# Performance work log

Hardware: AMD Instinct MI355X
Metric: run time of the kernel (lower is better)

## Reference

```python
import jax, jax.numpy as jnp
import numpy as np

TWO_PI = 2.0 * np.pi
ALPHA = 0.65
KSIZE = (3, 3, 3)   # (kOr, kH, kW)
ITERS = 1
BN_EPS = 1e-5


def _interp(v, dy, dx):
    """Bilinear sample of v[b,c,o, y+dy[o], x+dx[o]], border-clamped.
    v: [B,C,Or,H,W]; dy, dx: [Or] float per-orientation constant shifts."""
    H, W = v.shape[3], v.shape[4]
    y0 = jnp.floor(dy); fy = dy - y0; y0 = y0.astype(jnp.int32)
    iy = jnp.arange(H)[None, :] + y0[:, None]                      # [Or,H]
    g0 = jnp.take_along_axis(v, jnp.clip(iy, 0, H - 1)[None, None, :, :, None], axis=3)
    g1 = jnp.take_along_axis(v, jnp.clip(iy + 1, 0, H - 1)[None, None, :, :, None], axis=3)
    fyb = fy[None, None, :, None, None]
    v = (1.0 - fyb) * g0 + fyb * g1
    x0 = jnp.floor(dx); fx = dx - x0; x0 = x0.astype(jnp.int32)
    ix = jnp.arange(W)[None, :] + x0[:, None]                      # [Or,W]
    h0 = jnp.take_along_axis(v, jnp.clip(ix, 0, W - 1)[None, None, :, None, :], axis=4)
    h1 = jnp.take_along_axis(v, jnp.clip(ix + 1, 0, W - 1)[None, None, :, None, :], axis=4)
    fxb = fx[None, None, :, None, None]
    return (1.0 - fxb) * h0 + fxb * h1


def _convection(u, g0):
    """out[b,c,p] = u[b,c, p . g0[c]^{-1}] via trilinear resampling.
    Sample point: ((x,y) - R(theta - th0)@(x0,y0), theta - th0), theta periodic."""
    Or = u.shape[2]
    def one(uc, g):  # uc: [B,Or,H,W], g = (x0, y0, th0)
        x0, y0, th0 = g[0], g[1], g[2]
        t = th0 * Or / TWO_PI
        i = jnp.floor(t); f = t - i; i = i.astype(jnp.int32)
        # periodic linear interpolation along orientation axis
        v = (1.0 - f) * jnp.roll(uc, i, axis=1) + f * jnp.roll(uc, i + 1, axis=1)
        a = jnp.arange(Or, dtype=u.dtype) * (TWO_PI / Or) - th0
        dx = -(jnp.cos(a) * x0 - jnp.sin(a) * y0)
        dy = -(jnp.sin(a) * x0 + jnp.cos(a) * y0)
        return _interp(v[:, None], dy, dx)[:, 0]
    return jax.vmap(one, in_axes=(1, 0), out_axes=1)(u, g0)


def _se2_log(qx, qy, dth):
    """Exact SE(2) logarithm coordinates (c1,c2,c3) of group offset (qx,qy,dth)."""
    if abs(dth) < 1e-9:
        return qx, qy, dth
    h = 0.5 * dth
    cot = np.cos(h) / np.sin(h)
    return h * (qx * cot + qy), h * (-qx + qy * cot), dth


def _morph(u, metric, dilate):
    """Fractional morphological dilation (max of u(p.q) - k(q)) or erosion
    (min of u(p.q) + k(q)) with left-invariant Riemannian kernel
    k_c(q) = nu_a * d_c(q)^{2a/(2a-1)}, d_c^2 = (m0*c1)^2+(m1*c2)^2+(m2*c3)^2."""
    kOr, kH, kW = KSIZE
    Or = u.shape[2]
    thetas = jnp.arange(Or, dtype=u.dtype) * (TWO_PI / Or)
    p = 2.0 * ALPHA / (2.0 * ALPHA - 1.0)
    nu = (2.0 * ALPHA - 1.0) * (2.0 * ALPHA) ** (-p)
    out = None
    for qt in range(-(kOr // 2), kOr // 2 + 1):
        dth = qt * TWO_PI / Or
        for qy in range(-(kH // 2), kH // 2 + 1):
            for qx in range(-(kW // 2), kW // 2 + 1):
                c1, c2, c3 = _se2_log(float(qx), float(qy), dth)
                s = (metric[:, 0] * c1) ** 2 + (metric[:, 1] * c2) ** 2 + (metric[:, 2] * c3) ** 2
                k = nu * s ** (p / 2.0)                       # [C]
                # left-invariant shift: spatial offset rotated by theta_o
                dxo = jnp.cos(thetas) * qx - jnp.sin(thetas) * qy
                dyo = jnp.sin(thetas) * qx + jnp.cos(thetas) * qy
                val = _interp(jnp.roll(u, -qt, axis=2), dyo, dxo)
                kb = k[None, :, None, None, None]
                cand = val - kb if dilate else val + kb
                if out is None:
                    out = cand
                else:
                    out = jnp.maximum(out, cand) if dilate else jnp.minimum(out, cand)
    return out


def setup_inputs() -> dict:
    key = jax.random.key(0)
    ks = jax.random.split(key, 5)
    B, Cin, Cout, Or, H, W = 4, 8, 16, 8, 128, 128
    x = jax.random.normal(ks[0], (B, Cin, Or, H, W), dtype=jnp.float32)
    g0 = 0.5 * jax.random.normal(ks[1], (Cin, 3), dtype=jnp.float32)
    lo, hi = 1.4 / 3.0, 0.7 * 3.0   # reset_parameters range for metric params
    metric_dil = jax.random.uniform(ks[2], (Cin, 3), minval=lo, maxval=hi, dtype=jnp.float32)
    metric_ero = jax.random.uniform(ks[3], (Cin, 3), minval=lo, maxval=hi, dtype=jnp.float32)
    bound = 0.25  # kaiming_uniform(a=sqrt(5)) bound for [8,16] weight
    weight = jax.random.uniform(ks[4], (Cin, Cout), minval=-bound, maxval=bound, dtype=jnp.float32)
    gamma = jnp.ones((Cout,), jnp.float32)
    beta = jnp.zeros((Cout,), jnp.float32)
    return dict(x=x, g0=g0, metric_dil=metric_dil, metric_ero=metric_ero,
                weight=weight, gamma=gamma, beta=beta)


def reference(x, g0, metric_dil, metric_ero, weight, gamma, beta):
    u = x
    for _ in range(ITERS):
        u = _convection(u, g0)
        u = _morph(u, metric_dil, dilate=True)
        u = _morph(u, metric_ero, dilate=False)
    # channel mixing: [B,Cin,Or,H,W] x [Cin,Cout] -> [B,Cout,Or,H,W]
    y = jnp.einsum('bcohw,cd->bdohw', u, weight)
    # BatchNorm3d (training mode): per-channel stats over (B,Or,H,W)
    m = y.mean(axis=(0, 2, 3, 4), keepdims=True)
    v = y.var(axis=(0, 2, 3, 4), keepdims=True)
    yh = (y - m) * jax.lax.rsqrt(v + BN_EPS)
    return yh * gamma[None, :, None, None, None] + beta[None, :, None, None, None]
```

## Files before the change

### kernel.cpp

```cpp
#include <hip/hip_runtime.h>
#include <math.h>
#include <utility>

#define B 4
#define CIN 8
#define COUT 16
#define OR_ 8
#define H_ 128
#define W_ 128
#define HW 16384
#define PLANE HW
#define CH_STR (OR_*HW)
#define BATCH_STR (CIN*CH_STR)
#define NELEM (B*BATCH_STR)
#define NPOS (B*OR_*HW)
#define NB_RED 512

#define TILE 16
#define CBR 24
#define CB_S 29
#define CB_PL (CBR*CB_S)
#define DBR 20
#define DB_S 21
#define DB_PL (DBR*DB_S)

typedef __attribute__((ext_vector_type(4))) float f4;

struct Tables {
  float kdil[CIN][27];
  float kero[CIN][27];
  int   o1[CIN][OR_], o2[CIN][OR_];
  int   iy0[CIN][OR_], ix0[CIN][OR_];
  float w00[CIN][OR_], w01[CIN][OR_], w10[CIN][OR_], w11[CIN][OR_];
  float cf[CIN];
  int   iymin[CIN], iymax[CIN], ixmin[CIN], ixmax[CIN];
};

__host__ __device__ constexpr double m_cos(int o) {
  const double r = 0.70710678118654752440;
  const double t[8] = {1.0, r, 0.0, -r, -1.0, -r, 0.0, r};
  return t[o];
}
__host__ __device__ constexpr double m_sin(int o) {
  const double r = 0.70710678118654752440;
  const double t[8] = {0.0, r, 1.0, r, 0.0, -r, -1.0, -r};
  return t[o];
}
__host__ __device__ constexpr double tap_dx(int o, int j) {
  return m_cos(o)*(j % 3 - 1) - m_sin(o)*(j / 3 - 1);
}
__host__ __device__ constexpr double tap_dy(int o, int j) {
  return m_sin(o)*(j % 3 - 1) + m_cos(o)*(j / 3 - 1);
}
__host__ __device__ constexpr int ifloor(double v) {
  int i = (int)v;
  return ((double)i > v) ? i - 1 : i;
}
__host__ __device__ constexpr int tap_ix(int o, int j) { return ifloor(tap_dx(o, j)); }
__host__ __device__ constexpr int tap_iy(int o, int j) { return ifloor(tap_dy(o, j)); }
__host__ __device__ constexpr float tap_fx(int o, int j) { return (float)(tap_dx(o, j) - tap_ix(o, j)); }
__host__ __device__ constexpr float tap_fy(int o, int j) { return (float)(tap_dy(o, j) - tap_iy(o, j)); }
__host__ __device__ constexpr float corner_w(int o, int j, int dyb, int dxb) {
  float fy = tap_fy(o, j), fx = tap_fx(o, j);
  return (dyb ? fy : 1.0f - fy) * (dxb ? fx : 1.0f - fx);
}
__host__ __device__ constexpr int corner_r(int o, int j, int dyb) { return tap_iy(o, j) + dyb + 2; }
__host__ __device__ constexpr int corner_c(int o, int j, int i, int dxb) { return i + tap_ix(o, j) + dxb + 2; }
__host__ __device__ constexpr bool row_used(int o, int r) {
  for (int j = 0; j < 9; ++j)
    for (int dyb = 0; dyb < 2; ++dyb)
      for (int dxb = 0; dxb < 2; ++dxb)
        if (corner_w(o, j, dyb, dxb) != 0.0f && corner_r(o, j, dyb) == r)
          return true;
  return false;
}

template<int N> struct Rep {
  template<class F> __device__ __forceinline__ static void run(F&& f) {
    Rep<N-1>::run(f);
    f(std::integral_constant<int, N-1>{});
  }
};
template<> struct Rep<0> {
  template<class F> __device__ __forceinline__ static void run(F&&) {}
};


__global__ void precompute_kernel(const float* __restrict__ g0,
                                  const float* __restrict__ mdil,
                                  const float* __restrict__ mero,
                                  Tables* __restrict__ T) {
  const int t = threadIdx.x;
  const double TWO_PI = 6.283185307179586476925286766559;
  const double P  = 2.0*0.65/(2.0*0.65 - 1.0);
  const double NU = (2.0*0.65 - 1.0)*pow(2.0*0.65, -P);
  if (t < 432) {
    int which = t / 216;
    int r = t % 216;
    int c = r / 27;
    int j = r % 27;
    int qt = j/9 - 1;
    int qy = (j/3)%3 - 1;
    int qx = j%3 - 1;
    double dth = qt * (TWO_PI/OR_);
    double c1, c2, c3;
    if (qt == 0) { c1 = qx; c2 = qy; c3 = 0.0; }
    else {
      double h = 0.5*dth;
      double cot = cos(h)/sin(h);
      c1 = h*(qx*cot + qy);
      c2 = h*(-qx + qy*cot);
      c3 = dth;
    }
    const float* m = which ? mero : mdil;
    double a0 = (double)m[c*3+0]*c1;
    double a1 = (double)m[c*3+1]*c2;
    double a2 = (double)m[c*3+2]*c3;
    double s = a0*a0 + a1*a1 + a2*a2;
    float k = (float)(NU * pow(s, P*0.5));
    if (which) T->kero[c][j] = k; else T->kdil[c][j] = k;
  } else if (t >= 512 && t < 512 + CIN*OR_) {
    int r = t - 512;
    int c = r >> 3;
    int o = r & 7;
    float x0 = g0[c*3+0], y0 = g0[c*3+1], th0 = g0[c*3+2];
    float a = (float)(o*(TWO_PI/OR_)) - th0;
    float ca = cosf(a), sa = sinf(a);
    float dxv = -(ca*x0 - sa*y0);
    float dyv = -(sa*x0 + ca*y0);
    float fy0 = floorf(dyv), fx0 = floorf(dxv);
    float fy = dyv - fy0, fx = dxv - fx0;
    T->iy0[c][o] = (int)fy0;
    T->ix0[c][o] = (int)fx0;
    T->w00[c][o] = (1.f-fy)*(1.f-fx);
    T->w01[c][o] = (1.f-fy)*fx;
    T->w10[c][o] = fy*(1.f-fx);
    T->w11[c][o] = fy*fx;
    float tt = th0 * (float)(OR_/TWO_PI);
    float fi = floorf(tt);
    int ci = (int)fi;
    T->o1[c][o] = (o - ci) & 7;
    T->o2[c][o] = (o - ci - 1) & 7;
    if (o == 0) T->cf[c] = tt - fi;
  }
  __syncthreads();
  if (t < CIN) {
    int iymn = 999, iymx = -999, ixmn = 999, ixmx = -999;
    for (int o = 0; o < OR_; ++o) {
      iymn = min(iymn, T->iy0[t][o]); iymx = max(iymx, T->iy0[t][o]);
      ixmn = min(ixmn, T->ix0[t][o]); ixmx = max(ixmx, T->ix0[t][o]);
    }
    T->iymin[t] = iymn; T->iymax[t] = iymx;
    T->ixmin[t] = ixmn; T->ixmax[t] = ixmx;
  }
}

template<int O, int DIL, int PL, int RSTR>
__device__ __forceinline__ void morph_tile_lds(const float* __restrict__ sm,
                                               const float* __restrict__ kt,
                                               int row, int gc, float acc[4]) {
  Rep<3>::run([&](auto qc) {
    constexpr int qti = decltype(qc)::value;
    const float* p = sm + ((O + qti + 7) & 7) * PL + row * RSTR + gc;
    float win[5][8];
    Rep<5>::run([&](auto rc) {
      constexpr int r = decltype(rc)::value;
      if constexpr (row_used(O, r)) {
        #pragma unroll
        for (int k = 0; k < 8; ++k) win[r][k] = p[r*RSTR + k];
      }
    });
    Rep<9>::run([&](auto jc) {
      constexpr int j = decltype(jc)::value;
      float k = kt[qti*9 + j];
      float base = DIL ? -k : k;
      Rep<4>::run([&](auto ic) {
        constexpr int i = decltype(ic)::value;
        float v = base;
        Rep<4>::run([&](auto cc2) {
          constexpr int dyb = decltype(cc2)::value >> 1, dxb = decltype(cc2)::value & 1;
          constexpr float Wgt = corner_w(O, j, dyb, dxb);
          if constexpr (Wgt != 0.0f) {
            constexpr int R = corner_r(O, j, dyb);
            constexpr int C = corner_c(O, j, i, dxb);
            v = fmaf(Wgt, win[R][C], v);
          }
        });
        acc[i] = DIL ? fmaxf(acc[i], v) : fminf(acc[i], v);
      });
    });
  });
}

template<int O>
__device__ __forceinline__ void dil_wave(const float* __restrict__ cb, float* __restrict__ db,
                                         const float* __restrict__ kt, int lane) {
  {
    int rA = lane / 5, cA = (lane - rA*5) * 4;
    float acc[4] = {-INFINITY, -INFINITY, -INFINITY, -INFINITY};
    morph_tile_lds<O, 1, CB_PL, CB_S>(cb, kt, rA, cA, acc);
    float* d = db + O*DB_PL + rA*DB_S + cA;
    #pragma unroll
    for (int i = 0; i < 4; ++i) d[i] = acc[i];
  }
  if (lane < 36) {
    int g = lane + 64;
    int rB = g / 5, cB = (g - rB*5) * 4;
    float acc[4] = {-INFINITY, -INFINITY, -INFINITY, -INFINITY};
    morph_tile_lds<O, 1, CB_PL, CB_S>(cb, kt, rB, cB, acc);
    float* d = db + O*DB_PL + rB*DB_S + cB;
    #pragma unroll
    for (int i = 0; i < 4; ++i) d[i] = acc[i];
  }
}

template<int O>
__device__ __forceinline__ void ero_wave(const float* __restrict__ db, float* __restrict__ dst,
                                         const float* __restrict__ kt, int lane) {
  int pr = lane >> 2, pc = (lane & 3) * 4;
  float acc[4] = {INFINITY, INFINITY, INFINITY, INFINITY};
  morph_tile_lds<O, 0, DB_PL, DB_S>(db, kt, pr, pc, acc);
  f4 v = {acc[0], acc[1], acc[2], acc[3]};
  *(f4*)(dst + pr*W_ + pc) = v;
}

__global__ __launch_bounds__(512, 4)
void fused_kernel(const float* __restrict__ x, float* __restrict__ u3,
                  const Tables* __restrict__ T) {
  __shared__ float convbuf[8*CB_PL];
  __shared__ float dilbuf[8*DB_PL];

  int blk = blockIdx.x;
  int tx = blk & 7, ty = (blk >> 3) & 7, c = (blk >> 6) & 7, b = blk >> 9;
  int h0 = ty*TILE, w0 = tx*TILE;
  int t = threadIdx.x;
  int wid = t >> 6, lane = t & 63;

  {
    const int o = wid;
    const int iy0 = T->iy0[c][o], ix0 = T->ix0[c][o];
    const float w00 = T->w00[c][o], w01 = T->w01[c][o];
    const float w10 = T->w10[c][o], w11 = T->w11[c][o];
    const float cfv = T->cf[c];
    const float* p1 = x + b*BATCH_STR + c*CH_STR + T->o1[c][o]*PLANE;
    const float* p2 = x + b*BATCH_STR + c*CH_STR + T->o2[c][o]*PLANE;
    float* cbf = convbuf + o*CB_PL;
    bool interior = (h0 - 4 + T->iymin[c] >= 0) & (h0 + 20 + T->iymax[c] <= 127)
                  & (w0 - 4 + T->ixmin[c] >= 0) & (w0 + 20 + T->ixmax[c] <= 127)
                  & (h0 >= 16) & (h0 <= 96) & (w0 >= 16) & (w0 <= 96);
    if (interior) {
      #pragma unroll
      for (int it = 0; it < 3; ++it) {
        int q = lane + it*64;
        if (q < 144) {
          int r = q / 6;
          int cq = q - r*6;
          int iy = h0 - 4 + r + iy0;
          int ix = w0 - 4 + cq*4 + ix0;
          const float* q1 = p1 + iy*W_ + ix;
          const float* q2 = p2 + iy*W_ + ix;
          float a[5], bb[5], cc[5], dd[5];
          #pragma unroll
          for (int k = 0; k < 5; ++k) {
            a[k] = q1[k]; bb[k] = q1[W_+k]; cc[k] = q2[k]; dd[k] = q2[W_+k];
          }
          float* dst = cbf + r*CB_S + cq*4;
          #pragma unroll
          for (int i = 0; i < 4; ++i) {
            float v1 = w00*a[i] + w01*a[i+1] + w10*bb[i] + w11*bb[i+1];
            float v2 = w00*cc[i] + w01*cc[i+1] + w10*dd[i] + w11*dd[i+1];
            dst[i] = (1.0f - cfv)*v1 + cfv*v2;
          }
        }
      }
    } else {
      #pragma unroll
      for (int it = 0; it < 9; ++it) {
        int cell = lane + it*64;
        int r = cell / 24;
        int col = cell - r*24;
        int gh = min(max(h0 - 4 + r, 0), 127);
        int gw = min(max(w0 - 4 + col, 0), 127);
        int iy = gh + iy0, ix = gw + ix0;
        int r0 = min(max(iy, 0), 127), r1 = min(max(iy+1, 0), 127);
        int c0 = min(max(ix, 0), 127), c1 = min(max(ix+1, 0), 127);
        float v1 = w00*p1[r0*W_+c0] + w01*p1[r0*W_+c1] + w10*p1[r1*W_+c0] + w11*p1[r1*W_+c1];
        float v2 = w00*p2[r0*W_+c0] + w01*p2[r0*W_+c1] + w10*p2[r1*W_+c0] + w11*p2[r1*W_+c1];
        cbf[r*CB_S + col] = (1.0f - cfv)*v1 + cfv*v2;
      }
    }
  }
  __syncthreads();

  {
    const float* kt = T->kdil[c];
    switch (wid) {
      case 0: dil_wave<0>(convbuf, dilbuf, kt, lane); break;
      case 1: dil_wave<1>(convbuf, dilbuf, kt, lane); break;
      case 2: dil_wave<2>(convbuf, dilbuf, kt, lane); break;
      case 3: dil_wave<3>(convbuf, dilbuf, kt, lane); break;
      case 4: dil_wave<4>(convbuf, dilbuf, kt, lane); break;
      case 5: dil_wave<5>(convbuf, dilbuf, kt, lane); break;
      case 6: dil_wave<6>(convbuf, dilbuf, kt, lane); break;
      default: dil_wave<7>(convbuf, dilbuf, kt, lane); break;
    }
  }
  __syncthreads();

  if ((h0 == 0) | (h0 == 112) | (w0 == 0) | (w0 == 112)) {
    #pragma unroll
    for (int k2 = 0; k2 < 7; ++k2) {
      int i = t + k2*512;
      if (i < 3200) {
        int o = i / 400, rest = i - o*400;
        int row = rest / 20, col = rest - row*20;
        int vh = h0 - 2 + row, vw = w0 - 2 + col;
        int dr = min(max(vh, 0), 127) - vh;
        int dc = min(max(vw, 0), 127) - vw;
        if ((dr | dc) != 0) {
          dilbuf[o*DB_PL + row*DB_S + col] =
            dilbuf[o*DB_PL + (row + dr)*DB_S + col + dc];
        }
      }
    }
  }
  __syncthreads();

  {
    const float* kt = T->kero[c];
    float* dst = u3 + ((b*CIN + c)*OR_ + wid)*PLANE + h0*W_ + w0;
    switch (wid) {
      case 0: ero_wave<0>(dilbuf, dst, kt, lane); break;
      case 1: ero_wave<1>(dilbuf, dst, kt, lane); break;
      case 2: ero_wave<2>(dilbuf, dst, kt, lane); break;
      case 3: ero_wave<3>(dilbuf, dst, kt, lane); break;
      case 4: ero_wave<4>(dilbuf, dst, kt, lane); break;
      case 5: ero_wave<5>(dilbuf, dst, kt, lane); break;
      case 6: ero_wave<6>(dilbuf, dst, kt, lane); break;
      default: ero_wave<7>(dilbuf, dst, kt, lane); break;
    }
  }
}

__global__ void gram_kernel(const float* __restrict__ u, double* __restrict__ part) {
  int t4 = blockIdx.x*256 + threadIdx.x;
  int hw = (t4 & 4095) << 2;
  int o  = (t4 >> 12) & 7;
  int b  = t4 >> 15;
  const float* base = u + b*BATCH_STR + o*PLANE + hw;
  f4 v[8];
  #pragma unroll
  for (int c = 0; c < 8; c++) v[c] = *(const f4*)(base + c*CH_STR);
  float S[8], G[36];
  #pragma unroll
  for (int c = 0; c < 8; c++) S[c] = (v[c].x + v[c].y) + (v[c].z + v[c].w);
  {
    int t = 0;
    #pragma unroll
    for (int c = 0; c < 8; c++)
      #pragma unroll
      for (int c2 = c; c2 < 8; c2++) {
        G[t] = v[c].x*v[c2].x + v[c].y*v[c2].y + v[c].z*v[c2].z + v[c].w*v[c2].w;
        t++;
      }
  }
  __shared__ double lds[4][44];
  int lane = threadIdx.x & 63;
  int wave = threadIdx.x >> 6;
  for (int t = 0; t < 44; t++) {
    double vv = (double)((t < 8) ? S[t] : G[t-8]);
    for (int off = 32; off; off >>= 1) vv += __shfl_down(vv, off);
    if (lane == 0) lds[wave][t] = vv;
  }
  __syncthreads();
  if (threadIdx.x < 44) {
    part[blockIdx.x*44 + threadIdx.x] =
      lds[0][threadIdx.x] + lds[1][threadIdx.x] + lds[2][threadIdx.x] + lds[3][threadIdx.x];
  }
}

__global__ void stats_kernel(const double* __restrict__ part, const float* __restrict__ weight,
                             const float* __restrict__ gamma, const float* __restrict__ beta,
                             float* __restrict__ ss) {
  __shared__ double tot[44];
  int t = threadIdx.x;
  if (t < 352) {
    int cnt = t >> 3, j = t & 7;
    double s = 0.0;
    #pragma unroll 8
    for (int k = j; k < NB_RED; k += 8) s += part[k*44 + cnt];
    s += __shfl_down(s, 4);
    s += __shfl_down(s, 2);
    s += __shfl_down(s, 1);
    if (j == 0) tot[cnt] = s;
  }
  __syncthreads();
  if (t < 16) {
    double m = 0.0;
    for (int c = 0; c < 8; c++) m += (double)weight[c*COUT + t] * tot[c];
    double e2 = 0.0;
    int idx = 8;
    for (int c = 0; c < 8; c++)
      for (int c2 = c; c2 < 8; c2++) {
        double wp = (double)weight[c*COUT + t] * (double)weight[c2*COUT + t];
        e2 += (c2 == c ? 1.0 : 2.0) * wp * tot[idx];
        idx++;
      }
    double N = (double)NPOS;
    m /= N; e2 /= N;
    double var = e2 - m*m;
    double inv = rsqrt(var + 1e-5);
    float sc = (float)(inv * (double)gamma[t]);
    ss[t]      = sc;
    ss[16 + t] = beta[t] - (float)m * sc;
  }
}

__global__ void final_kernel(const float* __restrict__ u, const float* __restrict__ weight,
                             const float* __restrict__ ss, float* __restrict__ out) {
  __shared__ float Wsh[8][16];
  __shared__ float scale[16], shift[16];
  int t = threadIdx.x;
  if (t < 128) Wsh[t >> 4][t & 15] = weight[t];
  if (t < 16) { scale[t] = ss[t]; shift[t] = ss[16 + t]; }
  __syncthreads();
  int t4 = blockIdx.x*256 + threadIdx.x;
  int hw = (t4 & 4095) << 2;
  int o  = (t4 >> 12) & 7;
  int b  = t4 >> 15;
  const float* base = u + b*BATCH_STR + o*PLANE + hw;
  f4 v[8];
  #pragma unroll
  for (int c = 0; c < 8; c++) v[c] = *(const f4*)(base + c*CH_STR);
  float* ob = out + b*(COUT*CH_STR) + o*PLANE + hw;
  #pragma unroll
  for (int d = 0; d < 16; d++) {
    f4 y = {0.f, 0.f, 0.f, 0.f};
    #pragma unroll
    for (int c = 0; c < 8; c++) {
      float wv = Wsh[c][d];
      y.x = fmaf(v[c].x, wv, y.x);
      y.y = fmaf(v[c].y, wv, y.y);
      y.z = fmaf(v[c].z, wv, y.z);
      y.w = fmaf(v[c].w, wv, y.w);
    }
    float sc = scale[d], sh = shift[d];
    f4 r = { fmaf(y.x, sc, sh), fmaf(y.y, sc, sh), fmaf(y.z, sc, sh), fmaf(y.w, sc, sh) };
    *(f4*)(ob + d*CH_STR) = r;
  }
}

extern "C" void kernel_launch(void* const* d_in, const int* in_sizes, int n_in,
                              void* d_out, int out_size, void* d_ws, size_t ws_size,
                              hipStream_t stream) {
  const float* x      = (const float*)d_in[0];
  const float* g0     = (const float*)d_in[1];
  const float* mdil   = (const float*)d_in[2];
  const float* mero   = (const float*)d_in[3];
  const float* weight = (const float*)d_in[4];
  const float* gamma  = (const float*)d_in[5];
  const float* beta   = (const float*)d_in[6];
  float* out = (float*)d_out;

  char* ws = (char*)d_ws;
  Tables* T    = (Tables*)ws;
  float*  ss   = (float*)(ws + 8*1024);
  double* part = (double*)(ws + 16*1024);
  float*  u3   = (float*)(ws + (size_t)1*1024*1024);

  precompute_kernel<<<1, 1024, 0, stream>>>(g0, mdil, mero, T);
  fused_kernel<<<B*CIN*64, 512, 0, stream>>>(x, u3, T);
  gram_kernel<<<NB_RED, 256, 0, stream>>>(u3, part);
  stats_kernel<<<1, 384, 0, stream>>>(part, weight, gamma, beta, ss);
  final_kernel<<<NPOS/4/256, 256, 0, stream>>>(u3, weight, ss, out);
}
```

Before: 120.4 us.

## Fuse gram, stats and final kernels into one with grid-wide ticket sync

Merges the gram, stats and final kernels into a single tail kernel. The last block to arrive, detected by an atomic ticket, reduces the partial sums and publishes the BN scale and shift. All other blocks spin on a flag until it is set, then write their outputs from the u values already held in registers. This removes two launches and the second read of u3. It depends on all 512 blocks being co-resident (launch bounds of 2 blocks per CU) to avoid deadlock.

Result: slower. 178.8 us (+48.5%).

```diff
diff --git a/kernel.cpp b/kernel.cpp
--- a/kernel.cpp
+++ b/kernel.cpp
@@ -89,8 +89,10 @@
 __global__ void precompute_kernel(const float* __restrict__ g0,
                                   const float* __restrict__ mdil,
                                   const float* __restrict__ mero,
-                                  Tables* __restrict__ T) {
+                                  Tables* __restrict__ T,
+                                  unsigned int* __restrict__ sync) {
   const int t = threadIdx.x;
+  if (t == 1000) { sync[0] = 0u; sync[1] = 0u; }
   const double TWO_PI = 6.283185307179586476925286766559;
   const double P  = 2.0*0.65/(2.0*0.65 - 1.0);
   const double NU = (2.0*0.65 - 1.0)*pow(2.0*0.65, -P);
@@ -342,8 +344,17 @@
   }
 }
 
-__global__ void gram_kernel(const float* __restrict__ u, double* __restrict__ part) {
-  int t4 = blockIdx.x*256 + threadIdx.x;
+__global__ __launch_bounds__(256, 2)
+void tail_kernel(const float* __restrict__ u,
+                 const float* __restrict__ weight,
+                 const float* __restrict__ gamma,
+                 const float* __restrict__ beta,
+                 double* __restrict__ part,
+                 float* __restrict__ ss,
+                 unsigned int* __restrict__ sync,
+                 float* __restrict__ out) {
+  int t = threadIdx.x;
+  int t4 = blockIdx.x*256 + t;
   int hw = (t4 & 4095) << 2;
   int o  = (t4 >> 12) & 7;
   int b  = t4 >> 15;
@@ -351,87 +362,93 @@
   f4 v[8];
   #pragma unroll
   for (int c = 0; c < 8; c++) v[c] = *(const f4*)(base + c*CH_STR);
+
   float S[8], G[36];
   #pragma unroll
   for (int c = 0; c < 8; c++) S[c] = (v[c].x + v[c].y) + (v[c].z + v[c].w);
   {
-    int t = 0;
+    int q = 0;
     #pragma unroll
     for (int c = 0; c < 8; c++)
       #pragma unroll
       for (int c2 = c; c2 < 8; c2++) {
-        G[t] = v[c].x*v[c2].x + v[c].y*v[c2].y + v[c].z*v[c2].z + v[c].w*v[c2].w;
-        t++;
+        G[q] = v[c].x*v[c2].x + v[c].y*v[c2].y + v[c].z*v[c2].z + v[c].w*v[c2].w;
+        q++;
       }
   }
   __shared__ double lds[4][44];
-  int lane = threadIdx.x & 63;
-  int wave = threadIdx.x >> 6;
-  for (int t = 0; t < 44; t++) {
-    double vv = (double)((t < 8) ? S[t] : G[t-8]);
-    for (int off = 32; off; off >>= 1) vv += __shfl_down(vv, off);
-    if (lane == 0) lds[wave][t] = vv;
-  }
-  __syncthreads();
-  if (threadIdx.x < 44) {
-    part[blockIdx.x*44 + threadIdx.x] =
-      lds[0][threadIdx.x] + lds[1][threadIdx.x] + lds[2][threadIdx.x] + lds[3][threadIdx.x];
-  }
-}
-
-__global__ void stats_kernel(const double* __restrict__ part, const float* __restrict__ weight,
-                             const float* __restrict__ gamma, const float* __restrict__ beta,
-                             float* __restrict__ ss) {
-  __shared__ double tot[44];
-  int t = threadIdx.x;
-  if (t < 352) {
-    int cnt = t >> 3, j = t & 7;
-    double s = 0.0;
-    #pragma unroll 8
-    for (int k = j; k < NB_RED; k += 8) s += part[k*44 + cnt];
-    s += __shfl_down(s, 4);
-    s += __shfl_down(s, 2);
-    s += __shfl_down(s, 1);
-    if (j == 0) tot[cnt] = s;
-  }
-  __syncthreads();
-  if (t < 16) {
-    double m = 0.0;
-    for (int c = 0; c < 8; c++) m += (double)weight[c*COUT + t] * tot[c];
-    double e2 = 0.0;
-    int idx = 8;
-    for (int c = 0; c < 8; c++)
-      for (int c2 = c; c2 < 8; c2++) {
-        double wp = (double)weight[c*COUT + t] * (double)weight[c2*COUT + t];
-        e2 += (c2 == c ? 1.0 : 2.0) * wp * tot[idx];
-        idx++;
-      }
-    double N = (double)NPOS;
-    m /= N; e2 /= N;
-    double var = e2 - m*m;
-    double inv = rsqrt(var + 1e-5);
-    float sc = (float)(inv * (double)gamma[t]);
-    ss[t]      = sc;
-    ss[16 + t] = beta[t] - (float)m * sc;
-  }
-}
-
-__global__ void final_kernel(const float* __restrict__ u, const float* __restrict__ weight,
-                             const float* __restrict__ ss, float* __restrict__ out) {
   __shared__ float Wsh[8][16];
   __shared__ float scale[16], shift[16];
-  int t = threadIdx.x;
+  __shared__ unsigned int lastTicket;
+  int lane = t & 63;
+  int wave = t >> 6;
+  for (int q = 0; q < 44; q++) {
+    double vv = (double)((q < 8) ? S[q] : G[q-8]);
+    for (int off = 32; off; off >>= 1) vv += __shfl_down(vv, off);
+    if (lane == 0) lds[wave][q] = vv;
+  }
   if (t < 128) Wsh[t >> 4][t & 15] = weight[t];
-  if (t < 16) { scale[t] = ss[t]; shift[t] = ss[16 + t]; }
-  __syncthreads();
-  int t4 = blockIdx.x*256 + threadIdx.x;
-  int hw = (t4 & 4095) << 2;
-  int o  = (t4 >> 12) & 7;
-  int b  = t4 >> 15;
-  const float* base = u + b*BATCH_STR + o*PLANE + hw;
-  f4 v[8];
-  #pragma unroll
-  for (int c = 0; c < 8; c++) v[c] = *(const f4*)(base + c*CH_STR);
+  __syncthreads();
+  if (t < 44) {
+    part[blockIdx.x*44 + t] =
+      lds[0][t] + lds[1][t] + lds[2][t] + lds[3][t];
+  }
+  __threadfence();
+  __syncthreads();
+  if (t == 0) lastTicket = atomicAdd(&sync[0], 1u);
+  __syncthreads();
+
+  if (lastTicket == NB_RED - 1) {
+    __threadfence();
+    __shared__ double tot[44];
+    #pragma unroll
+    for (int base0 = 0; base0 < 64; base0 += 32) {
+      int cnt = base0 + (t >> 3);
+      int j = t & 7;
+      if (cnt < 44) {
+        double s = 0.0;
+        for (int k = j; k < NB_RED; k += 8) s += part[k*44 + cnt];
+        s += __shfl_down(s, 4);
+        s += __shfl_down(s, 2);
+        s += __shfl_down(s, 1);
+        if (j == 0) tot[cnt] = s;
+      }
+    }
+    __syncthreads();
+    if (t < 16) {
+      double m = 0.0;
+      for (int c = 0; c < 8; c++) m += (double)weight[c*COUT + t] * tot[c];
+      double e2 = 0.0;
+      int idx = 8;
+      for (int c = 0; c < 8; c++)
+        for (int c2 = c; c2 < 8; c2++) {
+          double wp = (double)weight[c*COUT + t] * (double)weight[c2*COUT + t];
+          e2 += (c2 == c ? 1.0 : 2.0) * wp * tot[idx];
+          idx++;
+        }
+      double N = (double)NPOS;
+      m /= N; e2 /= N;
+      double var = e2 - m*m;
+      double inv = rsqrt(var + 1e-5);
+      float sc = (float)(inv * (double)gamma[t]);
+      float sh = beta[t] - (float)m * sc;
+      ss[t]      = sc;
+      ss[16 + t] = sh;
+      scale[t] = sc;
+      shift[t] = sh;
+    }
+    __threadfence();
+    __syncthreads();
+    if (t == 0) atomicExch(&sync[1], 1u);
+  } else {
+    if (t == 0) {
+      while (atomicAdd(&sync[1], 0u) == 0u) __builtin_amdgcn_s_sleep(8);
+    }
+    __syncthreads();
+    if (t < 16) { scale[t] = ss[t]; shift[t] = ss[16 + t]; }
+  }
+  __syncthreads();
+
   float* ob = out + b*(COUT*CH_STR) + o*PLANE + hw;
   #pragma unroll
   for (int d = 0; d < 16; d++) {
@@ -464,13 +481,12 @@
 
   char* ws = (char*)d_ws;
   Tables* T    = (Tables*)ws;
+  unsigned int* sync = (unsigned int*)(ws + 6*1024);
   float*  ss   = (float*)(ws + 8*1024);
   double* part = (double*)(ws + 16*1024);
   float*  u3   = (float*)(ws + (size_t)1*1024*1024);
 
-  precompute_kernel<<<1, 1024, 0, stream>>>(g0, mdil, mero, T);
+  precompute_kernel<<<1, 1024, 0, stream>>>(g0, mdil, mero, T, sync);
   fused_kernel<<<B*CIN*64, 512, 0, stream>>>(x, u3, T);
-  gram_kernel<<<NB_RED, 256, 0, stream>>>(u3, part);
-  stats_kernel<<<1, 384, 0, stream>>>(part, weight, gamma, beta, ss);
-  final_kernel<<<NPOS/4/256, 256, 0, stream>>>(u3, weight, ss, out);
-}
+  tail_kernel<<<NB_RED, 256, 0, stream>>>(u3, weight, gamma, beta, part, ss, sync, out);
+}
```
